# Kernel optimization log

Measured on AMD Instinct MI355X. Metric: run time of the kernel, lower is better.

Reference implementation:

```python
import jax, jax.numpy as jnp
import numpy as np

NUM_NODES = 10000
WINDOW = 8
IN_C = 8
HID = 64
N_TOT = WINDOW * NUM_NODES
N_EDGES = 1280000
EPS = 1e-5


def setup_inputs() -> dict:
    key = jax.random.key(0)
    ks = jax.random.split(key, 12)
    s = 0.05
    X = jax.random.normal(ks[0], (N_TOT, IN_C), jnp.float32)
    edge_index = jax.random.randint(ks[1], (2, N_EDGES), 0, N_TOT, dtype=jnp.int32)
    edge_weight = jax.random.uniform(ks[2], (N_EDGES,), jnp.float32)
    return dict(
        X=X, edge_index=edge_index, edge_weight=edge_weight,
        w1=jax.random.normal(ks[3], (IN_C, HID), jnp.float32) * s, b1=jnp.zeros(HID, jnp.float32),
        w2=jax.random.normal(ks[4], (HID, HID), jnp.float32) * s, b2=jnp.zeros(HID, jnp.float32),
        g1=jnp.ones(HID, jnp.float32), be1=jnp.zeros(HID, jnp.float32),
        g2=jnp.ones(HID, jnp.float32), be2=jnp.zeros(HID, jnp.float32),
        wih1=jax.random.normal(ks[5], (4 * HID, 2 * HID), jnp.float32) * s,
        whh1=jax.random.normal(ks[6], (4 * HID, HID), jnp.float32) * s,
        bih1=jnp.zeros(4 * HID, jnp.float32), bhh1=jnp.zeros(4 * HID, jnp.float32),
        wih2=jax.random.normal(ks[7], (4 * HID, HID), jnp.float32) * s,
        whh2=jax.random.normal(ks[8], (4 * HID, HID), jnp.float32) * s,
        bih2=jnp.zeros(4 * HID, jnp.float32), bhh2=jnp.zeros(4 * HID, jnp.float32),
    )


def _gcn(x, src, dst, ew, w, b):
    h = x @ w
    deg = jax.ops.segment_sum(ew, dst, num_segments=N_TOT) + 1.0
    dinv = jax.lax.rsqrt(deg)
    norm = dinv[src] * ew * dinv[dst]                               # [E]
    agg = jax.ops.segment_sum(norm[:, None] * h[src], dst, num_segments=N_TOT)
    return agg + h * (dinv * dinv)[:, None] + b                      # self-loop term: h[i]/deg[i]


def _bn(x, g, b):
    # BatchNorm1d, training-mode batch statistics (biased variance)
    mu = x.mean(0)
    var = ((x - mu) ** 2).mean(0)
    return (x - mu) * jax.lax.rsqrt(var + EPS) * g + b


def _lstm(xs, wih, whh, bih, bhh):
    # xs: [T, B, F]; torch gate order i, f, g, o
    B = xs.shape[1]
    def step(carry, xt):
        h, c = carry
        z = xt @ wih.T + h @ whh.T + bih + bhh
        i, f, g, o = jnp.split(z, 4, axis=1)
        c = jax.nn.sigmoid(f) * c + jax.nn.sigmoid(i) * jnp.tanh(g)
        h = jax.nn.sigmoid(o) * jnp.tanh(c)
        return (h, c), h
    init = (jnp.zeros((B, HID), xs.dtype), jnp.zeros((B, HID), xs.dtype))
    (h, c), ys = jax.lax.scan(step, init, xs)
    return ys, h


def reference(X, edge_index, edge_weight, w1, b1, w2, b2, g1, be1, g2, be2,
              wih1, whh1, bih1, bhh1, wih2, whh2, bih2, bhh2):
    src, dst = edge_index[0], edge_index[1]
    # skip-feature S: [B*num_nodes, in_channels + window - 1]
    S = X.reshape(1, WINDOW, NUM_NODES, IN_C).transpose(0, 2, 1, 3).reshape(-1, WINDOW, IN_C)
    Sfeat = jnp.concatenate([S[:, 0, :], S[:, 1:, IN_C - 1]], axis=1)
    # two GCN layers (dropout omitted: deterministic baseline)
    x1 = _bn(jax.nn.relu(_gcn(X, src, dst, edge_weight, w1, b1)), g1, be1)
    x2 = _bn(jax.nn.relu(_gcn(x1, src, dst, edge_weight, w2, b2)), g2, be2)
    xc = jnp.concatenate([x1, x2], axis=1)                           # [N_TOT, 2H]
    xs = xc.reshape(1, WINDOW, NUM_NODES, 2 * HID).transpose(1, 0, 2, 3).reshape(WINDOW, -1, 2 * HID)
    ys, h1 = _lstm(xs, wih1, whh1, bih1, bhh1)
    ys2, h2 = _lstm(ys, wih2, whh2, bih2, bhh2)
    return jnp.concatenate([h1, h2, Sfeat], axis=1)                  # [num_nodes, 2H + IN_C + WINDOW - 1]
```

## Files before the change

kernel.cpp:

```cpp
#include <hip/hip_runtime.h>
#include <hip/hip_bf16.h>
#include <math.h>

#define NNODES 10000
#define NT     80000
#define NE     1280000
#define NBKT   625
#define CHUNK  5000
#define BNEPS  1e-5f

typedef __bf16 bf16x8 __attribute__((ext_vector_type(8)));
typedef float  f32x4  __attribute__((ext_vector_type(4)));
typedef float  f32x2  __attribute__((ext_vector_type(2)));

__device__ __forceinline__ float frcp(float x){ return __builtin_amdgcn_rcpf(x); }
__device__ __forceinline__ float fsig(float x){ return frcp(1.0f + __expf(-x)); }
__device__ __forceinline__ float ftanh(float x){ return 1.0f - 2.0f*frcp(1.0f + __expf(2.0f*x)); }
__device__ __forceinline__ float u2f(unsigned int u){ union{unsigned int u; float f;} c; c.u=u; return c.f; }
__device__ __forceinline__ unsigned int f2u(float f){ union{float f; unsigned int u;} c; c.f=f; return c.u; }
__device__ __forceinline__ unsigned short f2bu(float v){ __hip_bfloat16 h = __float2bfloat16(v); return *(unsigned short*)&h; }
__device__ __forceinline__ unsigned int pk2(float a, float b){ return (unsigned int)f2bu(a) | ((unsigned int)f2bu(b) << 16); }
__device__ __forceinline__ float dec15(unsigned int p){ return u2f((p & 0x7fffu) << 17); }

__global__ __launch_bounds__(256) void prep_w_kernel(
    const float* __restrict__ wih1, const float* __restrict__ whh1,
    const float* __restrict__ bih1, const float* __restrict__ bhh1,
    const float* __restrict__ wih2, const float* __restrict__ whh2,
    const float* __restrict__ bih2, const float* __restrict__ bhh2,
    const float* __restrict__ w1g, const float* __restrict__ w2g,
    unsigned int* __restrict__ W1f, unsigned int* __restrict__ W2f,
    float* __restrict__ bs1, float* __restrict__ bs2,
    unsigned int* __restrict__ W2g, unsigned int* __restrict__ W1g)
{
    int gid = blockIdx.x*256 + threadIdx.x;
    if (gid < 24576) {
        int i = gid & 3, lane = (gid>>2)&63, rest = gid>>8;
        int ks = rest % 6; rest /= 6;
        int nt = rest & 3, w = rest >> 2;
        int gate = nt*64 + w*16 + (lane & 15);
        int k = ks*32 + ((lane>>4)&3)*8 + 2*i;
        float v0 = (k     < 128) ? wih1[gate*128 + k]       : whh1[gate*64 + (k-128)];
        float v1 = (k + 1 < 128) ? wih1[gate*128 + k + 1]   : whh1[gate*64 + (k+1-128)];
        W1f[gid] = pk2(v0, v1);
    } else if (gid < 40960) {
        int r = gid - 24576;
        int i = r & 3, lane = (r>>2)&63, rest = r>>8;
        int ks = rest & 3; rest >>= 2;
        int nt = rest & 3, w = rest >> 2;
        int gate = nt*64 + w*16 + (lane & 15);
        int k = ks*32 + ((lane>>4)&3)*8 + 2*i;
        float v0 = (k     < 64) ? wih2[gate*64 + k]     : whh2[gate*64 + (k-64)];
        float v1 = (k + 1 < 64) ? wih2[gate*64 + k + 1] : whh2[gate*64 + (k+1-64)];
        W2f[r] = pk2(v0, v1);
    } else if (gid < 41216) {
        int j = gid - 40960; bs1[j] = bih1[j] + bhh1[j];
    } else if (gid < 41472) {
        int j = gid - 41216; bs2[j] = bih2[j] + bhh2[j];
    } else if (gid < 43520) {
        int r = gid - 41472;
        int i = r & 3, lane = (r>>2)&63, rest = r>>8;
        int ks = rest & 1, w = rest >> 1;
        int col = w*16 + (lane & 15);
        int k = ks*32 + ((lane>>4)&3)*8 + 2*i;
        W2g[r] = pk2(w2g[k*64 + col], w2g[(k+1)*64 + col]);
    } else if (gid < 44544) {
        int r = gid - 43520;
        int i = r & 3, lane = (r>>2)&63, w = r>>8;
        int col = w*16 + (lane & 15);
        int k = ((lane>>4)&3)*8 + 2*i;
        float v0 = (k     < 8) ? w1g[k*64 + col]     : 0.f;
        float v1 = (k + 1 < 8) ? w1g[(k+1)*64 + col] : 0.f;
        W1g[r] = pk2(v0, v1);
    }
}

__global__ __launch_bounds__(256) void sortA1_kernel(const int* __restrict__ dst,
                                                     int* __restrict__ histmat)
{
    __shared__ int h[NBKT];
    for (int i = threadIdx.x; i < NBKT; i += 256) h[i] = 0;
    __syncthreads();
    int base = blockIdx.x*CHUNK;
    for (int i = threadIdx.x; i < CHUNK; i += 256)
        atomicAdd(&h[dst[base + i] >> 7], 1);
    __syncthreads();
    for (int i = threadIdx.x; i < NBKT; i += 256)
        histmat[blockIdx.x*640 + i] = h[i];
}

__global__ __launch_bounds__(256) void sortA2a_kernel(const int* __restrict__ histmat,
                                                      int* __restrict__ offmatT,
                                                      int* __restrict__ binTotal)
{
    __shared__ int v[256];
    int b = blockIdx.x, t = threadIdx.x;
    int x = histmat[t*640 + b];
    v[t] = x;
    __syncthreads();
    for (int off = 1; off < 256; off <<= 1) {
        int y = (t >= off) ? v[t-off] : 0;
        __syncthreads();
        v[t] += y;
        __syncthreads();
    }
    offmatT[b*256 + t] = v[t] - x;
    if (t == 255) binTotal[b] = v[255];
}

__global__ __launch_bounds__(1024) void sortA2b_kernel(const int* __restrict__ binTotal,
                                                       int* __restrict__ bucketbase,
                                                       int* __restrict__ rowptr)
{
    __shared__ int part[1024];
    int t = threadIdx.x;
    int v = (t < NBKT) ? binTotal[t] : 0;
    part[t] = v;
    __syncthreads();
    for (int off = 1; off < 1024; off <<= 1) {
        int y = (t >= off) ? part[t-off] : 0;
        __syncthreads();
        part[t] += y;
        __syncthreads();
    }
    if (t < NBKT) bucketbase[t] = part[t] - v;
    if (t == 0) { bucketbase[NBKT] = NE; rowptr[NT] = NE; }
}

__global__ __launch_bounds__(256) void sortA3_kernel(const int* __restrict__ src,
                                                     const int* __restrict__ dst,
                                                     const float* __restrict__ ew,
                                                     const int* __restrict__ offmatT,
                                                     const int* __restrict__ bucketbase,
                                                     uint2* __restrict__ esort)
{
    __shared__ int cur[NBKT];
    int blk = blockIdx.x;
    for (int i = threadIdx.x; i < NBKT; i += 256)
        cur[i] = bucketbase[i] + offmatT[i*256 + blk];
    __syncthreads();
    int base = blk*CHUNK;
    for (int i = threadIdx.x; i < CHUNK; i += 256) {
        int e = base + i;
        int d = dst[e];
        int pos = atomicAdd(&cur[d >> 7], 1);
        uint2 r;
        r.x = (unsigned int)src[e] | ((unsigned int)(d & 127) << 17);
        r.y = f2u(ew[e]);
        esort[pos] = r;
    }
}

__global__ __launch_bounds__(256) void sortB1_kernel(const int* __restrict__ bucketbase,
                                                     const uint2* __restrict__ esort,
                                                     unsigned char* __restrict__ urank,
                                                     int* __restrict__ rowptr,
                                                     float* __restrict__ dinv)
{
    __shared__ int cnt[128];
    __shared__ float dg[128];
    __shared__ int ptr[128];
    int bin = blockIdx.x, t = threadIdx.x;
    if (t < 128) { cnt[t] = 0; dg[t] = 0.f; }
    __syncthreads();
    int base = bucketbase[bin], end = bucketbase[bin+1];
    for (int i = base + t; i < end; i += 256) {
        uint2 r = esort[i];
        int dl = (r.x >> 17) & 127;
        int rk = atomicAdd(&cnt[dl], 1);
        atomicAdd(&dg[dl], u2f(r.y));
        urank[i] = (unsigned char)rk;
    }
    __syncthreads();
    if (t < 128) ptr[t] = cnt[t];
    __syncthreads();
    for (int off = 1; off < 128; off <<= 1) {
        int y = (t >= off && t < 128) ? ptr[t-off] : 0;
        __syncthreads();
        if (t < 128) ptr[t] += y;
        __syncthreads();
    }
    if (t < 128) {
        rowptr[bin*128 + t] = base + ptr[t] - cnt[t];
        dinv[bin*128 + t]   = rsqrtf(dg[t] + 1.0f);
    }
}

__global__ __launch_bounds__(256) void sortB2_kernel(const int* __restrict__ bucketbase,
                                                     const uint2* __restrict__ esort,
                                                     const unsigned char* __restrict__ urank,
                                                     const int* __restrict__ rowptr,
                                                     const float* __restrict__ dinv,
                                                     unsigned int* __restrict__ epack)
{
    int bin = blockIdx.x;
    int base = bucketbase[bin], end = bucketbase[bin+1];
    for (int i = base + threadIdx.x; i < end; i += 256) {
        uint2 r = esort[i];
        int s = r.x & 0x1FFFF;
        int d = bin*128 + ((r.x >> 17) & 127);
        float w = u2f(r.y) * dinv[s];
        unsigned int p15 = (f2u(w) + (1u << 16)) >> 17;
        epack[rowptr[d] + (int)urank[i]] = ((unsigned int)s << 15) | p15;
    }
}

__global__ __launch_bounds__(256) void xconv_kernel(const float* __restrict__ X,
                                                    unsigned int* __restrict__ Xb)
{
    int gid = blockIdx.x*256 + threadIdx.x;
    if (gid >= NT*4) return;
    float2 v = *(const float2*)&X[(size_t)gid*2];
    Xb[gid] = pk2(v.x, v.y);
}

__global__ __launch_bounds__(256) void gather8_kernel(const int* __restrict__ rowptr,
                                                      const unsigned int* __restrict__ epack,
                                                      const uint4* __restrict__ Xb,
                                                      const float* __restrict__ dinv,
                                                      uint4* __restrict__ agg8b)
{
    int d = blockIdx.x*256 + threadIdx.x;
    if (d >= NT) return;
    int beg = rowptr[d], end = rowptr[d+1];
    float acc[8];
    #pragma unroll
    for (int k = 0; k < 8; ++k) acc[k] = 0.f;
    for (int i = beg; i < end; ++i) {
        unsigned int p = epack[i];
        float nrm = dec15(p);
        uint4 xv = Xb[p >> 15];
        unsigned int um[4] = {xv.x, xv.y, xv.z, xv.w};
        #pragma unroll
        for (int m = 0; m < 4; ++m) {
            acc[2*m]   = fmaf(nrm, u2f(um[m] << 16),         acc[2*m]);
            acc[2*m+1] = fmaf(nrm, u2f(um[m] & 0xffff0000u), acc[2*m+1]);
        }
    }
    float dv = dinv[d];
    uint4 xd = Xb[d];
    unsigned int ud[4] = {xd.x, xd.y, xd.z, xd.w};
    #pragma unroll
    for (int m = 0; m < 4; ++m) {
        acc[2*m]   = dv * fmaf(dv, u2f(ud[m] << 16),         acc[2*m]);
        acc[2*m+1] = dv * fmaf(dv, u2f(ud[m] & 0xffff0000u), acc[2*m+1]);
    }
    agg8b[d] = make_uint4(pk2(acc[0],acc[1]), pk2(acc[2],acc[3]),
                          pk2(acc[4],acc[5]), pk2(acc[6],acc[7]));
}

__global__ __launch_bounds__(256) void gemm8relu_kernel(const uint4* __restrict__ agg8b,
                                                        const unsigned int* __restrict__ W1g,
                                                        const float* __restrict__ b,
                                                        unsigned short* __restrict__ y,
                                                        float* __restrict__ sums)
{
    __shared__ __align__(16) unsigned short As[64][8];
    __shared__ float sm[256], sq[256];
    const int tid = threadIdx.x;
    const int w = tid >> 6, lane = tid & 63, lr = lane & 15, lg = lane >> 4;
    union { uint4 u; bf16x8 v; } bw; bw.u = ((const uint4*)W1g)[w*64 + lane];
    float bc = b[w*16 + lr];
    float s = 0.f, q = 0.f;
    for (int tile = blockIdx.x; tile < NT/64; tile += gridDim.x) {
        int rbase = tile*64;
        __syncthreads();
        if (tid < 64) *(uint4*)&As[tid][0] = agg8b[rbase + tid];
        __syncthreads();
        #pragma unroll
        for (int rt = 0; rt < 4; ++rt) {
            bf16x8 a = {};
            if (lg == 0) a = *(const bf16x8*)&As[rt*16 + lr][0];
            f32x4 acc = {0.f, 0.f, 0.f, 0.f};
            acc = __builtin_amdgcn_mfma_f32_16x16x32_bf16(a, bw.v, acc, 0, 0, 0);
            #pragma unroll
            for (int r = 0; r < 4; ++r) {
                float v = fmaxf(acc[r] + bc, 0.f);
                y[(size_t)(rbase + rt*16 + lg*4 + r)*64 + w*16 + lr] = f2bu(v);
                s += v; q += v*v;
            }
        }
    }
    sm[tid] = s; sq[tid] = q;
    __syncthreads();
    if (tid < 64) {
        int base = (tid >> 4)*64 + (tid & 15);
        atomicAdd(&sums[tid],      sm[base] + sm[base+16] + sm[base+32] + sm[base+48]);
        atomicAdd(&sums[64 + tid], sq[base] + sq[base+16] + sq[base+32] + sq[base+48]);
    }
}

__global__ __launch_bounds__(256) void xbn8_kernel(const unsigned int* __restrict__ y1,
                                                   const float* __restrict__ sums,
                                                   const float* __restrict__ g,
                                                   const float* __restrict__ be,
                                                   unsigned int* __restrict__ xcat,
                                                   unsigned int* __restrict__ x8)
{
    __shared__ float axs[64], bxs[64];
    int tid = threadIdx.x;
    if (tid < 64) {
        float mu  = sums[tid] * (1.0f/NT);
        float var = sums[64 + tid] * (1.0f/NT) - mu*mu;
        float a = rsqrtf(var + BNEPS) * g[tid];
        axs[tid] = a; bxs[tid] = be[tid] - mu*a;
    }
    __syncthreads();
    int gid = blockIdx.x*256 + tid;
    if (gid >= NT*16) return;
    int c4 = gid & 15, n = gid >> 4;
    int c0 = c4*4;
    uint2 yy = *(const uint2*)&y1[(size_t)n*32 + 2*c4];
    float v0 = fmaf(axs[c0+0], u2f(yy.x << 16),         bxs[c0+0]);
    float v1 = fmaf(axs[c0+1], u2f(yy.x & 0xffff0000u), bxs[c0+1]);
    float v2 = fmaf(axs[c0+2], u2f(yy.y << 16),         bxs[c0+2]);
    float v3 = fmaf(axs[c0+3], u2f(yy.y & 0xffff0000u), bxs[c0+3]);
    *(uint2*)&xcat[(size_t)n*64 + 2*c4] = make_uint2(pk2(v0, v1), pk2(v2, v3));
    int p8 = 0;
    p8 = __builtin_amdgcn_cvt_pk_fp8_f32(v0, v1, p8, false);
    p8 = __builtin_amdgcn_cvt_pk_fp8_f32(v2, v3, p8, true);
    x8[(size_t)n*16 + c4] = (unsigned int)p8;
}

__global__ __launch_bounds__(256) void gather64_kernel(const int* __restrict__ rowptr,
                                                       const unsigned int* __restrict__ epack,
                                                       const unsigned int* __restrict__ x8,
                                                       const float* __restrict__ dinv,
                                                       unsigned int* __restrict__ xcat)
{
    int lane = threadIdx.x & 63;
    int g = lane >> 3;
    int l = lane & 7;
    int gwave = blockIdx.x*4 + (threadIdx.x >> 6);
    int nwaves = gridDim.x*4;
    for (int d = gwave; d < NT; d += nwaves) {
        int beg = rowptr[d], end = rowptr[d+1];
        float a0=0.f,a1=0.f,a2=0.f,a3=0.f,a4=0.f,a5=0.f,a6=0.f,a7=0.f;
        for (int i = beg; i < end; i += 8) {
            int idx = i + g;
            bool valid = idx < end;
            unsigned int p = epack[valid ? idx : (end - 1)];
            float nrm = valid ? dec15(p) : 0.f;
            uint2 xv = *(const uint2*)&x8[(size_t)(p >> 15)*16 + 2*l];
            f32x2 q0 = __builtin_amdgcn_cvt_pk_f32_fp8((int)xv.x, false);
            f32x2 q1 = __builtin_amdgcn_cvt_pk_f32_fp8((int)xv.x, true);
            f32x2 q2 = __builtin_amdgcn_cvt_pk_f32_fp8((int)xv.y, false);
            f32x2 q3 = __builtin_amdgcn_cvt_pk_f32_fp8((int)xv.y, true);
            a0 = fmaf(nrm, q0[0], a0); a1 = fmaf(nrm, q0[1], a1);
            a2 = fmaf(nrm, q1[0], a2); a3 = fmaf(nrm, q1[1], a3);
            a4 = fmaf(nrm, q2[0], a4); a5 = fmaf(nrm, q2[1], a5);
            a6 = fmaf(nrm, q3[0], a6); a7 = fmaf(nrm, q3[1], a7);
        }
        #pragma unroll
        for (int off = 8; off < 64; off <<= 1) {
            a0 += __shfl_xor(a0, off); a1 += __shfl_xor(a1, off);
            a2 += __shfl_xor(a2, off); a3 += __shfl_xor(a3, off);
            a4 += __shfl_xor(a4, off); a5 += __shfl_xor(a5, off);
            a6 += __shfl_xor(a6, off); a7 += __shfl_xor(a7, off);
        }
        if (g == 0) {
            float dv = dinv[d];
            uint4 xd = *(const uint4*)&xcat[(size_t)d*64 + 4*l];
            float x0 = u2f(xd.x << 16), x1 = u2f(xd.x & 0xffff0000u);
            float x2 = u2f(xd.y << 16), x3 = u2f(xd.y & 0xffff0000u);
            float x4 = u2f(xd.z << 16), x5 = u2f(xd.z & 0xffff0000u);
            float x6 = u2f(xd.w << 16), x7 = u2f(xd.w & 0xffff0000u);
            a0 = dv * fmaf(dv, x0, a0); a1 = dv * fmaf(dv, x1, a1);
            a2 = dv * fmaf(dv, x2, a2); a3 = dv * fmaf(dv, x3, a3);
            a4 = dv * fmaf(dv, x4, a4); a5 = dv * fmaf(dv, x5, a5);
            a6 = dv * fmaf(dv, x6, a6); a7 = dv * fmaf(dv, x7, a7);
            *(uint4*)&xcat[(size_t)d*64 + 32 + 4*l] =
                make_uint4(pk2(a0,a1), pk2(a2,a3), pk2(a4,a5), pk2(a6,a7));
        }
    }
}

__global__ __launch_bounds__(256) void gemm64relu_kernel(const unsigned int* __restrict__ xcat,
                                                         const unsigned int* __restrict__ W2g,
                                                         const float* __restrict__ b,
                                                         unsigned short* __restrict__ y,
                                                         float* __restrict__ sums)
{
    __shared__ __align__(16) unsigned short As[64][72];
    __shared__ float sm[256], sq[256];
    const int tid = threadIdx.x;
    const int w = tid >> 6, lane = tid & 63, lr = lane & 15, lg = lane >> 4;
    union { uint4 u; bf16x8 v; } b0, b1;
    b0.u = ((const uint4*)W2g)[(w*2 + 0)*64 + lane];
    b1.u = ((const uint4*)W2g)[(w*2 + 1)*64 + lane];
    float bc = b[w*16 + lr];
    const int srow = tid >> 2, squad = tid & 3;
    float s = 0.f, q = 0.f;
    for (int tile = blockIdx.x; tile < NT/64; tile += gridDim.x) {
        int rbase = tile*64;
        __syncthreads();
        {
            const unsigned int* src = &xcat[(size_t)(rbase + srow)*64 + 32 + squad*8];
            unsigned int* dst = (unsigned int*)&As[srow][0] + squad*8;
            *(uint4*)(dst)     = *(const uint4*)(src);
            *(uint4*)(dst + 4) = *(const uint4*)(src + 4);
        }
        __syncthreads();
        #pragma unroll
        for (int rt = 0; rt < 4; ++rt) {
            bf16x8 a0 = *(const bf16x8*)&As[rt*16 + lr][lg*8];
            bf16x8 a1 = *(const bf16x8*)&As[rt*16 + lr][32 + lg*8];
            f32x4 acc = {0.f, 0.f, 0.f, 0.f};
            acc = __builtin_amdgcn_mfma_f32_16x16x32_bf16(a0, b0.v, acc, 0, 0, 0);
            acc = __builtin_amdgcn_mfma_f32_16x16x32_bf16(a1, b1.v, acc, 0, 0, 0);
            #pragma unroll
            for (int r = 0; r < 4; ++r) {
                float v = fmaxf(acc[r] + bc, 0.f);
                y[(size_t)(rbase + rt*16 + lg*4 + r)*64 + w*16 + lr] = f2bu(v);
                s += v; q += v*v;
            }
        }
    }
    sm[tid] = s; sq[tid] = q;
    __syncthreads();
    if (tid < 64) {
        int base = (tid >> 4)*64 + (tid & 15);
        atomicAdd(&sums[tid],      sm[base] + sm[base+16] + sm[base+32] + sm[base+48]);
        atomicAdd(&sums[64 + tid], sq[base] + sq[base+16] + sq[base+32] + sq[base+48]);
    }
}

#define LROW 328
__global__ __launch_bounds__(256, 2) void lstm_mfma_kernel(
    const unsigned int* __restrict__ xcat,
    const unsigned int* __restrict__ y2,
    const float* __restrict__ sums2, const float* __restrict__ g2,
    const float* __restrict__ be2,
    const unsigned int* __restrict__ W1f, const unsigned int* __restrict__ W2f,
    const float* __restrict__ bs1, const float* __restrict__ bs2,
    float* __restrict__ out)
{
    __shared__ __align__(16) unsigned short xb[16][LROW];
    const int tid  = threadIdx.x;
    const int w    = tid >> 6, lane = tid & 63;
    const int lr   = lane & 15;
    const int lg   = lane >> 4;
    const int nb0  = blockIdx.x * 16;

    uint4 w1f[4][6], w2f[4][4];
    {
        const uint4* p1 = (const uint4*)W1f;
        #pragma unroll
        for (int nt = 0; nt < 4; ++nt)
            #pragma unroll
            for (int ks = 0; ks < 6; ++ks)
                w1f[nt][ks] = p1[((w*4 + nt)*6 + ks)*64 + lane];
        const uint4* p2 = (const uint4*)W2f;
        #pragma unroll
        for (int nt = 0; nt < 4; ++nt)
            #pragma unroll
            for (int ks = 0; ks < 4; ++ks)
                w2f[nt][ks] = p2[((w*4 + nt)*4 + ks)*64 + lane];
    }
    float b1v[4], b2v[4];
    #pragma unroll
    for (int nt = 0; nt < 4; ++nt) {
        b1v[nt] = bs1[nt*64 + w*16 + lr];
        b2v[nt] = bs2[nt*64 + w*16 + lr];
    }

    const int sn = tid >> 4, k0 = (tid & 15)*8;
    float ax[8], bx[8];
    if (k0 >= 64) {
        #pragma unroll
        for (int j = 0; j < 8; ++j) {
            int c = k0 - 64 + j;
            float mu  = sums2[c] * (1.0f/NT);
            float var = sums2[64 + c] * (1.0f/NT) - mu*mu;
            float a = rsqrtf(var + BNEPS) * g2[c];
            ax[j] = a; bx[j] = be2[c] - mu*a;
        }
    }

    for (int i = tid; i < 16*24; i += 256) {
        int n = i / 24, kk = 128 + (i % 24)*8;
        uint4 z; z.x = z.y = z.z = z.w = 0u;
        *(uint4*)&xb[n][kk] = z;
    }

    auto stage = [&](int step) {
        size_t row = (size_t)(step*NNODES + nb0 + sn);
        uint4 raw;
        if (k0 < 64) {
            raw = *(const uint4*)&xcat[row*64 + (k0 >> 1)];
        } else {
            raw = *(const uint4*)&y2[row*32 + ((k0 - 64) >> 1)];
            unsigned int um[4] = {raw.x, raw.y, raw.z, raw.w};
            #pragma unroll
            for (int m = 0; m < 4; ++m) {
                float v0 = fmaf(ax[2*m],   u2f(um[m] << 16),         bx[2*m]);
                float v1 = fmaf(ax[2*m+1], u2f(um[m] & 0xffff0000u), bx[2*m+1]);
                um[m] = pk2(v0, v1);
            }
            raw.x = um[0]; raw.y = um[1]; raw.z = um[2]; raw.w = um[3];
        }
        *(uint4*)&xb[sn][k0] = raw;
    };
    stage(0);
    float c1[4] = {0.f,0.f,0.f,0.f}, c2[4] = {0.f,0.f,0.f,0.f};

    for (int step = 0; step < 8; ++step) {
        __syncthreads();

        f32x4 acc[4];
        #pragma unroll
        for (int nt = 0; nt < 4; ++nt) { acc[nt][0]=0.f; acc[nt][1]=0.f; acc[nt][2]=0.f; acc[nt][3]=0.f; }
        #pragma unroll
        for (int ks = 0; ks < 6; ++ks) {
            bf16x8 a = *(const bf16x8*)&xb[lr][ks*32 + lg*8];
            #pragma unroll
            for (int nt = 0; nt < 4; ++nt) {
                union { uint4 u; bf16x8 v; } wb; wb.u = w1f[nt][ks];
                acc[nt] = __builtin_amdgcn_mfma_f32_16x16x32_bf16(a, wb.v, acc[nt], 0, 0, 0);
            }
        }
        __syncthreads();

        #pragma unroll
        for (int r = 0; r < 4; ++r) {
            float zi = acc[0][r] + b1v[0];
            float zf = acc[1][r] + b1v[1];
            float zg = acc[2][r] + b1v[2];
            float zo = acc[3][r] + b1v[3];
            float c  = fsig(zf)*c1[r] + fsig(zi)*ftanh(zg);
            c1[r] = c;
            float hv = fsig(zo)*ftanh(c);
            int node = lg*4 + r;
            xb[node][128 + w*16 + lr] = f2bu(hv);
            if (step == 7) out[(size_t)(nb0 + node)*143 + w*16 + lr] = hv;
        }
        if (step < 7) stage(step + 1);
        __syncthreads();

        int rb = 192 + 64*((step+1)&1);
        int wb2 = 192 + 64*(step&1);
        #pragma unroll
        for (int nt = 0; nt < 4; ++nt) { acc[nt][0]=0.f; acc[nt][1]=0.f; acc[nt][2]=0.f; acc[nt][3]=0.f; }
        #pragma unroll
        for (int ks = 0; ks < 2; ++ks) {
            bf16x8 a = *(const bf16x8*)&xb[lr][128 + ks*32 + lg*8];
            #pragma unroll
            for (int nt = 0; nt < 4; ++nt) {
                union { uint4 u; bf16x8 v; } wbv; wbv.u = w2f[nt][ks];
                acc[nt] = __builtin_amdgcn_mfma_f32_16x16x32_bf16(a, wbv.v, acc[nt], 0, 0, 0);
            }
        }
        #pragma unroll
        for (int ks = 0; ks < 2; ++ks) {
            bf16x8 a = *(const bf16x8*)&xb[lr][rb + ks*32 + lg*8];
            #pragma unroll
            for (int nt = 0; nt < 4; ++nt) {
                union { uint4 u; bf16x8 v; } wbv; wbv.u = w2f[nt][2+ks];
                acc[nt] = __builtin_amdgcn_mfma_f32_16x16x32_bf16(a, wbv.v, acc[nt], 0, 0, 0);
            }
        }
        #pragma unroll
        for (int r = 0; r < 4; ++r) {
            float zi = acc[0][r] + b2v[0];
            float zf = acc[1][r] + b2v[1];
            float zg = acc[2][r] + b2v[2];
            float zo = acc[3][r] + b2v[3];
            float c  = fsig(zf)*c2[r] + fsig(zi)*ftanh(zg);
            c2[r] = c;
            float hv = fsig(zo)*ftanh(c);
            int node = lg*4 + r;
            xb[node][wb2 + w*16 + lr] = f2bu(hv);
            if (step == 7) out[(size_t)(nb0 + node)*143 + 64 + w*16 + lr] = hv;
        }
    }
}

__global__ __launch_bounds__(256) void sfeat_kernel(const float* __restrict__ X,
                                                    float* __restrict__ out)
{
    int gid = blockIdx.x*256 + threadIdx.x;
    if (gid >= NNODES*15) return;
    int n = gid/15, i = gid%15;
    float v = (i < 8) ? X[(size_t)n*8 + i]
                      : X[((size_t)(i-7)*NNODES + n)*8 + 7];
    out[(size_t)n*143 + 128 + i] = v;
}

extern "C" void kernel_launch(void* const* d_in, const int* in_sizes, int n_in,
                              void* d_out, int out_size, void* d_ws, size_t ws_size,
                              hipStream_t stream)
{
    (void)in_sizes; (void)n_in; (void)out_size; (void)ws_size;
    const float* X    = (const float*)d_in[0];
    const int*   ei   = (const int*)d_in[1];
    const float* ew   = (const float*)d_in[2];
    const float* w1   = (const float*)d_in[3];
    const float* b1   = (const float*)d_in[4];
    const float* w2   = (const float*)d_in[5];
    const float* b2   = (const float*)d_in[6];
    const float* g1   = (const float*)d_in[7];
    const float* be1  = (const float*)d_in[8];
    const float* g2   = (const float*)d_in[9];
    const float* be2  = (const float*)d_in[10];
    const float* wih1 = (const float*)d_in[11];
    const float* whh1 = (const float*)d_in[12];
    const float* bih1 = (const float*)d_in[13];
    const float* bhh1 = (const float*)d_in[14];
    const float* wih2 = (const float*)d_in[15];
    const float* whh2 = (const float*)d_in[16];
    const float* bih2 = (const float*)d_in[17];
    const float* bhh2 = (const float*)d_in[18];
    float* out = (float*)d_out;
    float* ws  = (float*)d_ws;

    const int* src = ei;
    const int* dst = ei + NE;

    float* sums      = ws;
    float* dinv      = ws + 256;
    int*   rowptr    = (int*)(ws + 80256);
    int*   binTotal  = (int*)(ws + 160260);
    int*   bucketbase= (int*)(ws + 160900);
    int*   histmat   = (int*)(ws + 161540);
    int*   offmatT   = (int*)(ws + 325380);
    unsigned char* urank = (unsigned char*)(ws + 485380);
    uint2* esort     = (uint2*)(ws + 805384);
    unsigned int* x8 = (unsigned int*)(ws + 805384);
    unsigned int* y2 = (unsigned int*)(ws + 805384);
    unsigned int* epack = (unsigned int*)(ws + 3365384);
    unsigned int* Xb = (unsigned int*)(ws + 4645384);
    uint4* agg8b     = (uint4*)(ws + 4965384);
    unsigned int* y1 = (unsigned int*)(ws + 5605384);
    unsigned int* xcat = (unsigned int*)(ws + 8165384);
    unsigned int* W1f  = (unsigned int*)(ws + 13285384);
    unsigned int* W2f  = W1f + 24576;
    float* bs1 = (float*)(W2f + 16384);
    float* bs2 = bs1 + 256;
    unsigned int* W2g  = (unsigned int*)(bs2 + 256);
    unsigned int* W1g  = W2g + 2048;

    hipMemsetAsync(ws, 0, 256 * 4, stream);

    prep_w_kernel<<<174, 256, 0, stream>>>(wih1,whh1,bih1,bhh1,
                                           wih2,whh2,bih2,bhh2,
                                           w1, w2,
                                           W1f,W2f,bs1,bs2,W2g,W1g);
    sortA1_kernel<<<256, 256, 0, stream>>>(dst, histmat);
    sortA2a_kernel<<<NBKT, 256, 0, stream>>>(histmat, offmatT, binTotal);
    sortA2b_kernel<<<1, 1024, 0, stream>>>(binTotal, bucketbase, rowptr);
    sortA3_kernel<<<256, 256, 0, stream>>>(src, dst, ew, offmatT, bucketbase, esort);
    sortB1_kernel<<<NBKT, 256, 0, stream>>>(bucketbase, esort, urank, rowptr, dinv);
    sortB2_kernel<<<NBKT, 256, 0, stream>>>(bucketbase, esort, urank, rowptr, dinv, epack);
    xconv_kernel<<<(NT*4+255)/256, 256, 0, stream>>>(X, Xb);

    gather8_kernel<<<(NT+255)/256, 256, 0, stream>>>(rowptr, epack, (const uint4*)Xb, dinv, agg8b);
    gemm8relu_kernel<<<320, 256, 0, stream>>>(agg8b, W1g, b1, (unsigned short*)y1, sums);

    xbn8_kernel<<<(NT*16+255)/256, 256, 0, stream>>>(y1, sums, g1, be1, xcat, x8);

    gather64_kernel<<<2048, 256, 0, stream>>>(rowptr, epack, x8, dinv, xcat);
    gemm64relu_kernel<<<320, 256, 0, stream>>>(xcat, W2g, b2, (unsigned short*)y2, sums + 128);

    lstm_mfma_kernel<<<NNODES/16, 256, 0, stream>>>(xcat, y2, sums + 128, g2, be2,
                                                    W1f, W2f, bs1, bs2, out);
    sfeat_kernel<<<(NNODES*15+255)/256, 256, 0, stream>>>(X, out);
}
```

Baseline: 192.6 us.

## Fuse X conversion into histogram, fuse edge packing with layer-1 gather, pair nodes in gather64

The X-to-bf16 conversion moves into the histogram kernel, and the edge-packing kernel now also performs the 8-channel neighbour gather. It keeps the packed edges of each bucket in shared memory and uses two threads per destination node. The 64-channel gather processes two destination nodes per wave so more loads are in flight. This removes two launches and a global round trip of the packed edges, at the cost of more registers and more imbalance between paired rows.

```diff
diff --git a/kernel.cpp b/kernel.cpp
--- a/kernel.cpp
+++ b/kernel.cpp
@@ -7,6 +7,7 @@
 #define NE     1280000
 #define NBKT   625
 #define CHUNK  5000
+#define EPB    3072
 #define BNEPS  1e-5f
 
 typedef __bf16 bf16x8 __attribute__((ext_vector_type(8)));
@@ -75,6 +76,8 @@
 }
 
 __global__ __launch_bounds__(256) void sortA1_kernel(const int* __restrict__ dst,
+                                                     const float* __restrict__ X,
+                                                     unsigned int* __restrict__ Xb,
                                                      int* __restrict__ histmat)
 {
     __shared__ int h[NBKT];
@@ -83,6 +86,11 @@
     int base = blockIdx.x*CHUNK;
     for (int i = threadIdx.x; i < CHUNK; i += 256)
         atomicAdd(&h[dst[base + i] >> 7], 1);
+    for (int i = threadIdx.x; i < 1250; i += 256) {
+        int gid = blockIdx.x*1250 + i;
+        float2 v = *(const float2*)&X[(size_t)gid*2];
+        Xb[gid] = pk2(v.x, v.y);
+    }
     __syncthreads();
     for (int i = threadIdx.x; i < NBKT; i += 256)
         histmat[blockIdx.x*640 + i] = h[i];
@@ -185,48 +193,42 @@
     }
 }
 
-__global__ __launch_bounds__(256) void sortB2_kernel(const int* __restrict__ bucketbase,
-                                                     const uint2* __restrict__ esort,
-                                                     const unsigned char* __restrict__ urank,
-                                                     const int* __restrict__ rowptr,
-                                                     const float* __restrict__ dinv,
-                                                     unsigned int* __restrict__ epack)
-{
+__global__ __launch_bounds__(256) void sortB2g8_kernel(const int* __restrict__ bucketbase,
+                                                       const uint2* __restrict__ esort,
+                                                       const unsigned char* __restrict__ urank,
+                                                       const int* __restrict__ rowptr,
+                                                       const float* __restrict__ dinv,
+                                                       unsigned int* __restrict__ epack,
+                                                       const uint4* __restrict__ Xb,
+                                                       uint4* __restrict__ agg8b)
+{
+    __shared__ unsigned int eld[EPB];
     int bin = blockIdx.x;
     int base = bucketbase[bin], end = bucketbase[bin+1];
-    for (int i = base + threadIdx.x; i < end; i += 256) {
-        uint2 r = esort[i];
+    int cnt = end - base;
+    for (int i = threadIdx.x; i < cnt; i += 256) {
+        uint2 r = esort[base + i];
         int s = r.x & 0x1FFFF;
         int d = bin*128 + ((r.x >> 17) & 127);
         float w = u2f(r.y) * dinv[s];
         unsigned int p15 = (f2u(w) + (1u << 16)) >> 17;
-        epack[rowptr[d] + (int)urank[i]] = ((unsigned int)s << 15) | p15;
-    }
-}
-
-__global__ __launch_bounds__(256) void xconv_kernel(const float* __restrict__ X,
-                                                    unsigned int* __restrict__ Xb)
-{
-    int gid = blockIdx.x*256 + threadIdx.x;
-    if (gid >= NT*4) return;
-    float2 v = *(const float2*)&X[(size_t)gid*2];
-    Xb[gid] = pk2(v.x, v.y);
-}
-
-__global__ __launch_bounds__(256) void gather8_kernel(const int* __restrict__ rowptr,
-                                                      const unsigned int* __restrict__ epack,
-                                                      const uint4* __restrict__ Xb,
-                                                      const float* __restrict__ dinv,
-                                                      uint4* __restrict__ agg8b)
-{
-    int d = blockIdx.x*256 + threadIdx.x;
-    if (d >= NT) return;
-    int beg = rowptr[d], end = rowptr[d+1];
+        unsigned int pv = ((unsigned int)s << 15) | p15;
+        int pos = rowptr[d] + (int)urank[base + i];
+        epack[pos] = pv;
+        int lpos = pos - base;
+        if (lpos < EPB) eld[lpos] = pv;
+    }
+    __syncthreads();
+    int t = threadIdx.x;
+    int dl = t >> 1, par = t & 1;
+    int d = bin*128 + dl;
+    int beg = rowptr[d], endd = rowptr[d+1];
     float acc[8];
     #pragma unroll
     for (int k = 0; k < 8; ++k) acc[k] = 0.f;
-    for (int i = beg; i < end; ++i) {
-        unsigned int p = epack[i];
+    for (int i = beg + par; i < endd; i += 2) {
+        int lpos = i - base;
+        unsigned int p = (lpos < EPB) ? eld[lpos] : epack[i];
         float nrm = dec15(p);
         uint4 xv = Xb[p >> 15];
         unsigned int um[4] = {xv.x, xv.y, xv.z, xv.w};
@@ -236,16 +238,20 @@
             acc[2*m+1] = fmaf(nrm, u2f(um[m] & 0xffff0000u), acc[2*m+1]);
         }
     }
-    float dv = dinv[d];
-    uint4 xd = Xb[d];
-    unsigned int ud[4] = {xd.x, xd.y, xd.z, xd.w};
     #pragma unroll
-    for (int m = 0; m < 4; ++m) {
-        acc[2*m]   = dv * fmaf(dv, u2f(ud[m] << 16),         acc[2*m]);
-        acc[2*m+1] = dv * fmaf(dv, u2f(ud[m] & 0xffff0000u), acc[2*m+1]);
-    }
-    agg8b[d] = make_uint4(pk2(acc[0],acc[1]), pk2(acc[2],acc[3]),
-                          pk2(acc[4],acc[5]), pk2(acc[6],acc[7]));
+    for (int k = 0; k < 8; ++k) acc[k] += __shfl_xor(acc[k], 1);
+    if (par == 0) {
+        float dv = dinv[d];
+        uint4 xd = Xb[d];
+        unsigned int ud[4] = {xd.x, xd.y, xd.z, xd.w};
+        #pragma unroll
+        for (int m = 0; m < 4; ++m) {
+            acc[2*m]   = dv * fmaf(dv, u2f(ud[m] << 16),         acc[2*m]);
+            acc[2*m+1] = dv * fmaf(dv, u2f(ud[m] & 0xffff0000u), acc[2*m+1]);
+        }
+        agg8b[d] = make_uint4(pk2(acc[0],acc[1]), pk2(acc[2],acc[3]),
+                              pk2(acc[4],acc[5]), pk2(acc[6],acc[7]));
+    }
 }
 
 __global__ __launch_bounds__(256) void gemm8relu_kernel(const uint4* __restrict__ agg8b,
@@ -332,23 +338,43 @@
     int l = lane & 7;
     int gwave = blockIdx.x*4 + (threadIdx.x >> 6);
     int nwaves = gridDim.x*4;
-    for (int d = gwave; d < NT; d += nwaves) {
-        int beg = rowptr[d], end = rowptr[d+1];
+    for (int dp = gwave; dp < NT/2; dp += nwaves) {
+        int dA = dp*2, dB = dA + 1;
+        int begA = rowptr[dA], endA = rowptr[dA+1];
+        int begB = endA, endB = rowptr[dB+1];
+        int nA = endA - begA, nB = endB - begB;
+        int n = nA > nB ? nA : nB;
+        int clA = (endA > begA) ? endA - 1 : 0;
+        int clB = (endB > begB) ? endB - 1 : 0;
         float a0=0.f,a1=0.f,a2=0.f,a3=0.f,a4=0.f,a5=0.f,a6=0.f,a7=0.f;
-        for (int i = beg; i < end; i += 8) {
-            int idx = i + g;
-            bool valid = idx < end;
-            unsigned int p = epack[valid ? idx : (end - 1)];
-            float nrm = valid ? dec15(p) : 0.f;
-            uint2 xv = *(const uint2*)&x8[(size_t)(p >> 15)*16 + 2*l];
-            f32x2 q0 = __builtin_amdgcn_cvt_pk_f32_fp8((int)xv.x, false);
-            f32x2 q1 = __builtin_amdgcn_cvt_pk_f32_fp8((int)xv.x, true);
-            f32x2 q2 = __builtin_amdgcn_cvt_pk_f32_fp8((int)xv.y, false);
-            f32x2 q3 = __builtin_amdgcn_cvt_pk_f32_fp8((int)xv.y, true);
-            a0 = fmaf(nrm, q0[0], a0); a1 = fmaf(nrm, q0[1], a1);
-            a2 = fmaf(nrm, q1[0], a2); a3 = fmaf(nrm, q1[1], a3);
-            a4 = fmaf(nrm, q2[0], a4); a5 = fmaf(nrm, q2[1], a5);
-            a6 = fmaf(nrm, q3[0], a6); a7 = fmaf(nrm, q3[1], a7);
+        float b0=0.f,b1=0.f,b2=0.f,b3=0.f,b4=0.f,b5=0.f,b6=0.f,b7=0.f;
+        for (int i = 0; i < n; i += 8) {
+            int iA = begA + i + g;
+            bool vA = iA < endA;
+            unsigned int pA = epack[vA ? iA : clA];
+            float nrmA = vA ? dec15(pA) : 0.f;
+            int iB = begB + i + g;
+            bool vB = iB < endB;
+            unsigned int pB = epack[vB ? iB : clB];
+            float nrmB = vB ? dec15(pB) : 0.f;
+            uint2 xvA = *(const uint2*)&x8[(size_t)(pA >> 15)*16 + 2*l];
+            uint2 xvB = *(const uint2*)&x8[(size_t)(pB >> 15)*16 + 2*l];
+            f32x2 qa0 = __builtin_amdgcn_cvt_pk_f32_fp8((int)xvA.x, false);
+            f32x2 qa1 = __builtin_amdgcn_cvt_pk_f32_fp8((int)xvA.x, true);
+            f32x2 qa2 = __builtin_amdgcn_cvt_pk_f32_fp8((int)xvA.y, false);
+            f32x2 qa3 = __builtin_amdgcn_cvt_pk_f32_fp8((int)xvA.y, true);
+            a0 = fmaf(nrmA, qa0[0], a0); a1 = fmaf(nrmA, qa0[1], a1);
+            a2 = fmaf(nrmA, qa1[0], a2); a3 = fmaf(nrmA, qa1[1], a3);
+            a4 = fmaf(nrmA, qa2[0], a4); a5 = fmaf(nrmA, qa2[1], a5);
+            a6 = fmaf(nrmA, qa3[0], a6); a7 = fmaf(nrmA, qa3[1], a7);
+            f32x2 qb0 = __builtin_amdgcn_cvt_pk_f32_fp8((int)xvB.x, false);
+            f32x2 qb1 = __builtin_amdgcn_cvt_pk_f32_fp8((int)xvB.x, true);
+            f32x2 qb2 = __builtin_amdgcn_cvt_pk_f32_fp8((int)xvB.y, false);
+            f32x2 qb3 = __builtin_amdgcn_cvt_pk_f32_fp8((int)xvB.y, true);
+            b0 = fmaf(nrmB, qb0[0], b0); b1 = fmaf(nrmB, qb0[1], b1);
+            b2 = fmaf(nrmB, qb1[0], b2); b3 = fmaf(nrmB, qb1[1], b3);
+            b4 = fmaf(nrmB, qb2[0], b4); b5 = fmaf(nrmB, qb2[1], b5);
+            b6 = fmaf(nrmB, qb3[0], b6); b7 = fmaf(nrmB, qb3[1], b7);
         }
         #pragma unroll
         for (int off = 8; off < 64; off <<= 1) {
@@ -356,20 +382,36 @@
             a2 += __shfl_xor(a2, off); a3 += __shfl_xor(a3, off);
             a4 += __shfl_xor(a4, off); a5 += __shfl_xor(a5, off);
             a6 += __shfl_xor(a6, off); a7 += __shfl_xor(a7, off);
+            b0 += __shfl_xor(b0, off); b1 += __shfl_xor(b1, off);
+            b2 += __shfl_xor(b2, off); b3 += __shfl_xor(b3, off);
+            b4 += __shfl_xor(b4, off); b5 += __shfl_xor(b5, off);
+            b6 += __shfl_xor(b6, off); b7 += __shfl_xor(b7, off);
         }
         if (g == 0) {
-            float dv = dinv[d];
-            uint4 xd = *(const uint4*)&xcat[(size_t)d*64 + 4*l];
-            float x0 = u2f(xd.x << 16), x1 = u2f(xd.x & 0xffff0000u);
-            float x2 = u2f(xd.y << 16), x3 = u2f(xd.y & 0xffff0000u);
-            float x4 = u2f(xd.z << 16), x5 = u2f(xd.z & 0xffff0000u);
-            float x6 = u2f(xd.w << 16), x7 = u2f(xd.w & 0xffff0000u);
-            a0 = dv * fmaf(dv, x0, a0); a1 = dv * fmaf(dv, x1, a1);
-            a2 = dv * fmaf(dv, x2, a2); a3 = dv * fmaf(dv, x3, a3);
-            a4 = dv * fmaf(dv, x4, a4); a5 = dv * fmaf(dv, x5, a5);
-            a6 = dv * fmaf(dv, x6, a6); a7 = dv * fmaf(dv, x7, a7);
-            *(uint4*)&xcat[(size_t)d*64 + 32 + 4*l] =
+            float dvA = dinv[dA];
+            uint4 xdA = *(const uint4*)&xcat[(size_t)dA*64 + 4*l];
+            a0 = dvA * fmaf(dvA, u2f(xdA.x << 16),         a0);
+            a1 = dvA * fmaf(dvA, u2f(xdA.x & 0xffff0000u), a1);
+            a2 = dvA * fmaf(dvA, u2f(xdA.y << 16),         a2);
+            a3 = dvA * fmaf(dvA, u2f(xdA.y & 0xffff0000u), a3);
+            a4 = dvA * fmaf(dvA, u2f(xdA.z << 16),         a4);
+            a5 = dvA * fmaf(dvA, u2f(xdA.z & 0xffff0000u), a5);
+            a6 = dvA * fmaf(dvA, u2f(xdA.w << 16),         a6);
+            a7 = dvA * fmaf(dvA, u2f(xdA.w & 0xffff0000u), a7);
+            *(uint4*)&xcat[(size_t)dA*64 + 32 + 4*l] =
                 make_uint4(pk2(a0,a1), pk2(a2,a3), pk2(a4,a5), pk2(a6,a7));
+            float dvB = dinv[dB];
+            uint4 xdB = *(const uint4*)&xcat[(size_t)dB*64 + 4*l];
+            b0 = dvB * fmaf(dvB, u2f(xdB.x << 16),         b0);
+            b1 = dvB * fmaf(dvB, u2f(xdB.x & 0xffff0000u), b1);
+            b2 = dvB * fmaf(dvB, u2f(xdB.y << 16),         b2);
+            b3 = dvB * fmaf(dvB, u2f(xdB.y & 0xffff0000u), b3);
+            b4 = dvB * fmaf(dvB, u2f(xdB.z << 16),         b4);
+            b5 = dvB * fmaf(dvB, u2f(xdB.z & 0xffff0000u), b5);
+            b6 = dvB * fmaf(dvB, u2f(xdB.w << 16),         b6);
+            b7 = dvB * fmaf(dvB, u2f(xdB.w & 0xffff0000u), b7);
+            *(uint4*)&xcat[(size_t)dB*64 + 32 + 4*l] =
+                make_uint4(pk2(b0,b1), pk2(b2,b3), pk2(b4,b5), pk2(b6,b7));
         }
     }
 }
@@ -644,15 +686,14 @@
                                            wih2,whh2,bih2,bhh2,
                                            w1, w2,
                                            W1f,W2f,bs1,bs2,W2g,W1g);
-    sortA1_kernel<<<256, 256, 0, stream>>>(dst, histmat);
+    sortA1_kernel<<<256, 256, 0, stream>>>(dst, X, Xb, histmat);
     sortA2a_kernel<<<NBKT, 256, 0, stream>>>(histmat, offmatT, binTotal);
     sortA2b_kernel<<<1, 1024, 0, stream>>>(binTotal, bucketbase, rowptr);
     sortA3_kernel<<<256, 256, 0, stream>>>(src, dst, ew, offmatT, bucketbase, esort);
     sortB1_kernel<<<NBKT, 256, 0, stream>>>(bucketbase, esort, urank, rowptr, dinv);
-    sortB2_kernel<<<NBKT, 256, 0, stream>>>(bucketbase, esort, urank, rowptr, dinv, epack);
-    xconv_kernel<<<(NT*4+255)/256, 256, 0, stream>>>(X, Xb);
-
-    gather8_kernel<<<(NT+255)/256, 256, 0, stream>>>(rowptr, epack, (const uint4*)Xb, dinv, agg8b);
+    sortB2g8_kernel<<<NBKT, 256, 0, stream>>>(bucketbase, esort, urank, rowptr, dinv,
+                                              epack, (const uint4*)Xb, agg8b);
+
     gemm8relu_kernel<<<320, 256, 0, stream>>>(agg8b, W1g, b1, (unsigned short*)y1, sums);
 
     xbn8_kernel<<<(NT*16+255)/256, 256, 0, stream>>>(y1, sums, g1, be1, xcat, x8);
```

After: 179.7 us. -6.7%, faster.
